# Kernel tuning notes

Hardware: AMD Instinct MI355X
Metric: run time of the kernel (lower is better)

The kernel has to match this reference:

```python
import jax, jax.numpy as jnp
import numpy as np

B, T, D, H = 2, 2048, 1024, 16
HD = D // H  # head dim = 64; rope half-dim = 32


def setup_inputs() -> dict:
    key = jax.random.key(0)
    ks = jax.random.split(key, 8)
    x = jax.random.normal(ks[0], (B, T, D), dtype=jnp.float32)
    # additive causal mask (upper triangle = -inf-like), as typically passed in
    mask = jnp.triu(jnp.full((T, T), -1e9, dtype=jnp.float32), k=1)
    # standard RoPE angles: theta = pos / 10000^(2i/hd)
    inv_freq = 1.0 / (10000.0 ** (np.arange(0, HD, 2, dtype=np.float32) / HD))
    ang = np.arange(T, dtype=np.float32)[:, None] * inv_freq[None, :]  # [T, HD//2]
    cos = jnp.asarray(np.cos(ang), dtype=jnp.float32)
    sin = jnp.asarray(np.sin(ang), dtype=jnp.float32)
    s = 1.0 / np.sqrt(D)
    Wq = jax.random.normal(ks[1], (D, D), dtype=jnp.float32) * s
    bq = jnp.zeros((D,), dtype=jnp.float32)
    Wk = jax.random.normal(ks[2], (D, D), dtype=jnp.float32) * s
    Wv = jax.random.normal(ks[3], (D, D), dtype=jnp.float32) * s
    bv = jnp.zeros((D,), dtype=jnp.float32)
    Wo = jax.random.normal(ks[4], (D, D), dtype=jnp.float32) * s
    bo = jnp.zeros((D,), dtype=jnp.float32)
    return {"x": x, "mask": mask, "cos": cos, "sin": sin, "Wq": Wq, "bq": bq,
            "Wk": Wk, "Wv": Wv, "bv": bv, "Wo": Wo, "bo": bo}


def _apply_rope(t, cos, sin):
    # t: [B, T, H, HD]; cos/sin: [T, HD//2]; complex multiply on (even, odd) pairs
    t = t.reshape(B, T, H, HD // 2, 2)
    t0, t1 = t[..., 0], t[..., 1]
    c = cos[None, :, None, :]
    s = sin[None, :, None, :]
    out = jnp.stack([t0 * c - t1 * s, t0 * s + t1 * c], axis=-1)
    return out.reshape(B, T, H, HD)


def reference(x, mask, cos, sin, Wq, bq, Wk, Wv, bv, Wo, bo):
    scale = float(HD) ** (-0.25)
    q = (x @ Wq.T + bq).reshape(B, T, H, HD)
    k = (x @ Wk.T).reshape(B, T, H, HD)  # key proj has no bias
    v = (x @ Wv.T + bv).reshape(B, T, H, HD)
    q = _apply_rope(q, cos, sin)
    k = _apply_rope(k, cos, sin)
    q = q.transpose(0, 2, 1, 3) * scale  # [B,H,T,HD]
    k = k.transpose(0, 2, 1, 3) * scale
    v = v.transpose(0, 2, 1, 3)
    qk = jnp.einsum("bhtd,bhsd->bhts", q, k) + mask  # [B,H,T,T]
    qk = qk.astype(jnp.float32)
    w = jax.nn.softmax(qk, axis=-1).astype(q.dtype)
    wv = jnp.einsum("bhts,bhsd->bhtd", w, v)
    wv = wv.transpose(0, 2, 1, 3).reshape(B, T, D)
    out = wv @ Wo.T + bo
    return out, qk
```

## Files before the change

### kernel.cpp

```cpp
#include <hip/hip_runtime.h>
#include <math.h>

#define Tc 2048
#define Dc 1024
#define Hc 16
#define HDc 64
#define BT 4096
#define SCALE 0.35355339059327379f

typedef _Float16 f16;
typedef __attribute__((ext_vector_type(4))) _Float16 f16x4;
typedef __attribute__((ext_vector_type(8))) _Float16 f16x8;
typedef __attribute__((ext_vector_type(4))) float f32x4;

__device__ __forceinline__ void gload16(const f16* g, f16* l)
{
    __builtin_amdgcn_global_load_lds(
        (const __attribute__((address_space(1))) void*)g,
        (__attribute__((address_space(3))) void*)l, 16, 0, 0);
}

template <int C>
__device__ __forceinline__ float fdpp(float x)
{
    return __int_as_float(__builtin_amdgcn_update_dpp(
        0, __float_as_int(x), C, 0xF, 0xF, true));
}
__device__ __forceinline__ float rmax16(float v)
{
    v = fmaxf(v, fdpp<0xB1>(v));
    v = fmaxf(v, fdpp<0x4E>(v));
    v = fmaxf(v, fdpp<0x124>(v));
    v = fmaxf(v, fdpp<0x128>(v));
    return v;
}
__device__ __forceinline__ float rsum16(float v)
{
    v += fdpp<0xB1>(v);
    v += fdpp<0x4E>(v);
    v += fdpp<0x124>(v);
    v += fdpp<0x128>(v);
    return v;
}

__global__ __launch_bounds__(256)
void cast_kernel(const float* __restrict__ x,
                 const float* __restrict__ Wq, const float* __restrict__ Wk,
                 const float* __restrict__ Wv, const float* __restrict__ Wo,
                 f16* __restrict__ xh,
                 f16* __restrict__ Wqh, f16* __restrict__ Wkh,
                 f16* __restrict__ Wvh, f16* __restrict__ Woh)
{
    const int u = blockIdx.y;
    const float* s; f16* d;
    if (u < 4) { s = x + (size_t)u * (1u << 20); d = xh + (size_t)u * (1u << 20); }
    else switch (u) {
        case 4:  s = Wq; d = Wqh; break;
        case 5:  s = Wk; d = Wkh; break;
        case 6:  s = Wv; d = Wvh; break;
        default: s = Wo; d = Woh; break;
    }
    int i = blockIdx.x * 256 + threadIdx.x;
    float4 v = ((const float4*)s)[i];
    f16x4 o = {(f16)v.x, (f16)v.y, (f16)v.z, (f16)v.w};
    ((f16x4*)d)[i] = o;
}

#define GEMM_BODY(Aptr, Bptr)                                                        \
    __shared__ f16 As[2][128 * 64];                                                  \
    __shared__ f16 Bs[2][64 * 64];                                                   \
    const int tid = threadIdx.x;                                                     \
    const int w = tid >> 6, l = tid & 63;                                            \
    const int lr = l & 15, lq = l >> 4;                                              \
    const int m0 = blockIdx.y * 128, n0 = blockIdx.x * 64;                           \
    const int srow8 = l >> 3, sslot = l & 7;                                         \
    f32x4 acc[2][4] = {};                                                            \
    auto STAGE = [&](int b, int k0) {                                                \
        _Pragma("unroll")                                                            \
        for (int c = 0; c < 6; c++) {                                                \
            int chunk = w * 6 + c;                                                   \
            if (chunk < 16) {                                                        \
                int row = chunk * 8 + srow8;                                         \
                int col = (sslot ^ (row & 7)) * 8;                                   \
                gload16(&Aptr[(size_t)(m0 + row) * Dc + k0 + col],                   \
                        &As[b][chunk * 512]);                                        \
            } else {                                                                 \
                int row = (chunk - 16) * 8 + srow8;                                  \
                int col = (sslot ^ (row & 7)) * 8;                                   \
                gload16(&Bptr[(size_t)(n0 + row) * Dc + k0 + col],                   \
                        &Bs[b][(chunk - 16) * 512]);                                 \
            }                                                                        \
        }                                                                            \
    };                                                                               \
    STAGE(0, 0);                                                                     \
    __syncthreads();                                                                 \
    int cur = 0;                                                                     \
    for (int k0 = 0; k0 < Dc; k0 += 64) {                                            \
        if (k0 + 64 < Dc) STAGE(cur ^ 1, k0 + 64);                                   \
        _Pragma("unroll")                                                            \
        for (int kk = 0; kk < 2; kk++) {                                             \
            f16x8 af[2], bf[4];                                                      \
            _Pragma("unroll")                                                        \
            for (int mi = 0; mi < 2; mi++) {                                         \
                int row = 32 * w + 16 * mi + lr;                                     \
                int bo = (lq * 16 + kk * 64) ^ ((row & 7) << 4);                     \
                af[mi] = *(const f16x8*)((const char*)&As[cur][0] + row * 128 + bo); \
            }                                                                        \
            _Pragma("unroll")                                                        \
            for (int ni = 0; ni < 4; ni++) {                                         \
                int row = 16 * ni + lr;                                              \
                int bo = (lq * 16 + kk * 64) ^ ((row & 7) << 4);                     \
                bf[ni] = *(const f16x8*)((const char*)&Bs[cur][0] + row * 128 + bo); \
            }                                                                        \
            _Pragma("unroll")                                                        \
            for (int mi = 0; mi < 2; mi++)                                           \
                _Pragma("unroll")                                                    \
                for (int ni = 0; ni < 4; ni++)                                       \
                    acc[mi][ni] = __builtin_amdgcn_mfma_f32_16x16x32_f16(            \
                        af[mi], bf[ni], acc[mi][ni], 0, 0, 0);                       \
        }                                                                            \
        __syncthreads();                                                             \
        cur ^= 1;                                                                    \
    }

__global__ __launch_bounds__(256, 3)
void qkv_proj_kernel(const f16* __restrict__ xh,
                     const f16* __restrict__ Wqh, const f16* __restrict__ Wkh,
                     const f16* __restrict__ Wvh,
                     const float* __restrict__ bq, const float* __restrict__ bv,
                     f16* __restrict__ qh, f16* __restrict__ kh, f16* __restrict__ vh,
                     const float* __restrict__ cosp, const float* __restrict__ sinp)
{
    const int mode = blockIdx.z;
    const f16* W = (mode == 0) ? Wqh : (mode == 1 ? Wkh : Wvh);
    const float* bias = (mode == 0) ? bq : (mode == 2 ? bv : nullptr);
    f16* dst = (mode == 0) ? qh : (mode == 1 ? kh : vh);

    GEMM_BODY(xh, W)

    #pragma unroll
    for (int mi = 0; mi < 2; mi++) {
        #pragma unroll
        for (int ni = 0; ni < 4; ni++) {
            #pragma unroll
            for (int i = 0; i < 4; i++) {
                int gm = m0 + 32 * w + 16 * mi + lq * 4 + i;
                int gn = n0 + 16 * ni + lr;
                float v = acc[mi][ni][i];
                if (bias) v += bias[gn];
                int b = gm >> 11, t = gm & 2047;
                int h = gn >> 6, d = gn & 63;
                if (mode != 2) {
                    float pv = __shfl_xor(v, 1, 64);
                    int p = d >> 1;
                    float c = cosp[t * 32 + p], s = sinp[t * 32 + p];
                    v = (d & 1) ? (pv * s + v * c) : (v * c - pv * s);
                    v *= SCALE;
                }
                dst[((size_t)(b * Hc + h) * Tc + t) * HDc + d] = (f16)v;
            }
        }
    }
}

__global__ __launch_bounds__(256, 3)
void out_proj_kernel(const f16* __restrict__ A, const f16* __restrict__ W,
                     const float* __restrict__ bias, float* __restrict__ out)
{
    GEMM_BODY(A, W)

    #pragma unroll
    for (int mi = 0; mi < 2; mi++)
        #pragma unroll
        for (int ni = 0; ni < 4; ni++)
            #pragma unroll
            for (int i = 0; i < 4; i++) {
                int gm = m0 + 32 * w + 16 * mi + lq * 4 + i;
                int gn = n0 + 16 * ni + lr;
                out[(size_t)gm * Dc + gn] = acc[mi][ni][i] + bias[gn];
            }
}

__global__ __launch_bounds__(256, 6)
void flash_kernel(const f16* __restrict__ qh, const f16* __restrict__ kh,
                  const f16* __restrict__ vh, f16* __restrict__ wvh,
                  float* __restrict__ qk)
{
    const int z = blockIdx.y;
    const int t0 = (gridDim.x - 1 - blockIdx.x) * 64;
    const int tid = threadIdx.x;
    const int w = tid >> 6, l = tid & 63;
    const int lr = l & 15, lq = l >> 4;

    __shared__ f16 Ks[64][64];
    __shared__ f16 VsT[64][68];
    __shared__ f16 Ps[64][68];

    const f16* Qg = qh + (size_t)z * Tc * HDc;
    const f16* Kg = kh + (size_t)z * Tc * HDc;
    const f16* Vg = vh + (size_t)z * Tc * HDc;
    float* C = qk + (size_t)z * Tc * Tc;

    f16x8 aq[2];
    #pragma unroll
    for (int ks = 0; ks < 2; ks++)
        aq[ks] = *(const f16x8*)&Qg[(size_t)(t0 + 16 * w + lr) * HDc + lq * 8 + 32 * ks];

    f32x4 O[4] = {};
    float mrow[4], lrow[4];
    #pragma unroll
    for (int i = 0; i < 4; i++) { mrow[i] = -1e30f; lrow[i] = 0.f; }

    const int srow8 = l >> 3, sslot = l & 7;

    for (int s0 = 0; s0 <= t0; s0 += 64) {
        __syncthreads();

        #pragma unroll
        for (int c = 0; c < 2; c++) {
            int chunk = w * 2 + c;
            int row = chunk * 8 + srow8;
            int col = (sslot ^ (row & 7)) * 8;
            gload16(&Kg[(size_t)(s0 + row) * HDc + col],
                    (f16*)((char*)&Ks[0][0] + chunk * 1024));
        }
        {
            const f16* vp = &Vg[(size_t)(s0 + l) * HDc + w * 16];
            f16x8 v0 = *(const f16x8*)vp;
            f16x8 v1 = *(const f16x8*)(vp + 8);
            #pragma unroll
            for (int j = 0; j < 8; j++) {
                VsT[w * 16 + j][l]     = v0[j];
                VsT[w * 16 + 8 + j][l] = v1[j];
            }
        }
        __syncthreads();

        f32x4 S[4] = {};
        __builtin_amdgcn_s_setprio(1);
        #pragma unroll
        for (int ks = 0; ks < 2; ks++) {
            #pragma unroll
            for (int ni = 0; ni < 4; ni++) {
                int krow = 16 * ni + lr;
                int bo = (lq * 16 + ks * 64) ^ ((krow & 7) << 4);
                f16x8 bk = *(const f16x8*)((const char*)&Ks[0][0] + krow * 128 + bo);
                S[ni] = __builtin_amdgcn_mfma_f32_16x16x32_f16(aq[ks], bk, S[ni], 0, 0, 0);
            }
        }
        __builtin_amdgcn_s_setprio(0);

        if (s0 == t0) {
            #pragma unroll
            for (int ni = 0; ni < 4; ni++)
                #pragma unroll
                for (int i = 0; i < 4; i++) {
                    int tg = t0 + 16 * w + lq * 4 + i;
                    int sg = s0 + 16 * ni + lr;
                    if (sg > tg) S[ni][i] = -1e9f;
                }
        }

        #pragma unroll
        for (int ni = 0; ni < 4; ni++)
            #pragma unroll
            for (int i = 0; i < 4; i++) {
                int tg = t0 + 16 * w + lq * 4 + i;
                int sg = s0 + 16 * ni + lr;
                C[(size_t)tg * Tc + sg] = S[ni][i];
            }

        #pragma unroll
        for (int i = 0; i < 4; i++) {
            float v = fmaxf(fmaxf(S[0][i], S[1][i]), fmaxf(S[2][i], S[3][i]));
            v = rmax16(v);
            float mnew = fmaxf(mrow[i], v);
            float alpha = __expf(mrow[i] - mnew);
            mrow[i] = mnew;
            float rs = 0.f;
            #pragma unroll
            for (int ni = 0; ni < 4; ni++) {
                float p = __expf(S[ni][i] - mnew);
                S[ni][i] = p;
                rs += p;
            }
            rs = rsum16(rs);
            lrow[i] = lrow[i] * alpha + rs;
            #pragma unroll
            for (int ni = 0; ni < 4; ni++) O[ni][i] *= alpha;
        }

        #pragma unroll
        for (int ni = 0; ni < 4; ni++)
            #pragma unroll
            for (int i = 0; i < 4; i++)
                Ps[16 * w + lq * 4 + i][16 * ni + lr] = (f16)S[ni][i];

        __builtin_amdgcn_s_setprio(1);
        #pragma unroll
        for (int ks = 0; ks < 2; ks++) {
            f16x8 ap = *(const f16x8*)&Ps[16 * w + lr][lq * 8 + 32 * ks];
            #pragma unroll
            for (int ni = 0; ni < 4; ni++) {
                f16x8 bv = *(const f16x8*)&VsT[16 * ni + lr][lq * 8 + 32 * ks];
                O[ni] = __builtin_amdgcn_mfma_f32_16x16x32_f16(ap, bv, O[ni], 0, 0, 0);
            }
        }
        __builtin_amdgcn_s_setprio(0);
    }

    const int b = z >> 4, h = z & 15;
    #pragma unroll
    for (int ni = 0; ni < 4; ni++)
        #pragma unroll
        for (int i = 0; i < 4; i++) {
            int tg = t0 + 16 * w + lq * 4 + i;
            int d = 16 * ni + lr;
            float o = O[ni][i] / lrow[i];
            wvh[((size_t)(b * Tc + tg)) * Dc + h * HDc + d] = (f16)o;
        }

    {
        int r = t0 + (tid >> 2);
        int n4 = (Tc - t0 - 64) >> 2;
        float4 mv; mv.x = mv.y = mv.z = mv.w = -1e9f;
        float4* rowp = (float4*)(C + (size_t)r * Tc + t0 + 64);
        for (int c = (tid & 3); c < n4; c += 4) rowp[c] = mv;
    }
}

extern "C" void kernel_launch(void* const* d_in, const int* in_sizes, int n_in,
                              void* d_out, int out_size, void* d_ws, size_t ws_size,
                              hipStream_t stream)
{
    const float* x    = (const float*)d_in[0];
    const float* cosp = (const float*)d_in[2];
    const float* sinp = (const float*)d_in[3];
    const float* Wq   = (const float*)d_in[4];
    const float* bq   = (const float*)d_in[5];
    const float* Wk   = (const float*)d_in[6];
    const float* Wv   = (const float*)d_in[7];
    const float* bv   = (const float*)d_in[8];
    const float* Wo   = (const float*)d_in[9];
    const float* bo   = (const float*)d_in[10];

    float* out = (float*)d_out;
    float* qk  = out + (size_t)BT * Dc;

    f16* ws  = (f16*)d_ws;
    f16* xh  = ws;
    f16* Wqh = xh  + (size_t)BT * Dc;
    f16* Wkh = Wqh + (size_t)Dc * Dc;
    f16* Wvh = Wkh + (size_t)Dc * Dc;
    f16* Woh = Wvh + (size_t)Dc * Dc;
    f16* qh  = Woh + (size_t)Dc * Dc;
    f16* kh  = qh  + (size_t)BT * Dc;
    f16* vh  = kh  + (size_t)BT * Dc;
    f16* wvh = vh  + (size_t)BT * Dc;

    dim3 blk(256);

    cast_kernel<<<dim3(1024, 8), blk, 0, stream>>>(
        x, Wq, Wk, Wv, Wo, xh, Wqh, Wkh, Wvh, Woh);

    qkv_proj_kernel<<<dim3(Dc / 64, BT / 128, 3), blk, 0, stream>>>(
        xh, Wqh, Wkh, Wvh, bq, bv, qh, kh, vh, cosp, sinp);

    flash_kernel<<<dim3(Tc / 64, 32), blk, 0, stream>>>(qh, kh, vh, wvh, qk);

    out_proj_kernel<<<dim3(Dc / 64, BT / 128), blk, 0, stream>>>(wvh, Woh, bo, out);
}
```

Before: 726.7 us.

## Split qk score output into a separate coalesced score kernel

Removes the strided scalar writes of the full qk score matrix and the masked-region fill from the flash kernel. A new score kernel recomputes Q·K^T in 128x128 tiles and stores it with vectorized f32x4 writes laid out along the key dimension. Tiles above the diagonal only write the mask constant. This recomputes the QK matmul, roughly doubling that compute, in exchange for a lighter flash loop and better-coalesced stores of the 512MB score tensor.

```diff
diff --git a/kernel.cpp b/kernel.cpp
--- a/kernel.cpp
+++ b/kernel.cpp
@@ -181,10 +181,90 @@
             }
 }
 
+__global__ __launch_bounds__(256, 4)
+void score_kernel(const f16* __restrict__ qh, const f16* __restrict__ kh,
+                  float* __restrict__ qk)
+{
+    const int z = blockIdx.z;
+    const int s0 = blockIdx.x * 128;
+    const int t0 = blockIdx.y * 128;
+    const int tid = threadIdx.x;
+    float* C = qk + (size_t)z * Tc * Tc;
+
+    if (s0 > t0) {
+        int r = t0 + (tid >> 1);
+        float* rowp = C + (size_t)r * Tc + s0 + (tid & 1) * 64;
+        f32x4 mv = {-1e9f, -1e9f, -1e9f, -1e9f};
+        #pragma unroll
+        for (int j = 0; j < 16; j++)
+            ((f32x4*)rowp)[j] = mv;
+        return;
+    }
+
+    __shared__ f16 KT[128 * 64];
+    __shared__ f16 QT[128 * 64];
+
+    const int w = tid >> 6, l = tid & 63;
+    const int lr = l & 15, lq = l >> 4;
+    const int srow8 = l >> 3, sslot = l & 7;
+
+    const f16* Qg = qh + (size_t)z * Tc * HDc;
+    const f16* Kg = kh + (size_t)z * Tc * HDc;
+
+    #pragma unroll
+    for (int c = 0; c < 8; c++) {
+        int chunk = w * 8 + c;
+        int row = (chunk & 15) * 8 + srow8;
+        int col = (sslot ^ (row & 7)) * 8;
+        if (chunk < 16)
+            gload16(&Kg[(size_t)(s0 + row) * HDc + col], &KT[chunk * 512]);
+        else
+            gload16(&Qg[(size_t)(t0 + row) * HDc + col], &QT[(chunk - 16) * 512]);
+    }
+    __syncthreads();
+
+    f32x4 acc[2][8] = {};
+    #pragma unroll
+    for (int kk = 0; kk < 2; kk++) {
+        f16x8 af[2], bf[8];
+        #pragma unroll
+        for (int mi = 0; mi < 2; mi++) {
+            int row = 32 * w + 16 * mi + lr;
+            int bo = (lq * 16 + kk * 64) ^ ((row & 7) << 4);
+            af[mi] = *(const f16x8*)((const char*)&KT[0] + row * 128 + bo);
+        }
+        #pragma unroll
+        for (int ni = 0; ni < 8; ni++) {
+            int row = 16 * ni + lr;
+            int bo = (lq * 16 + kk * 64) ^ ((row & 7) << 4);
+            bf[ni] = *(const f16x8*)((const char*)&QT[0] + row * 128 + bo);
+        }
+        #pragma unroll
+        for (int mi = 0; mi < 2; mi++)
+            #pragma unroll
+            for (int ni = 0; ni < 8; ni++)
+                acc[mi][ni] = __builtin_amdgcn_mfma_f32_16x16x32_f16(
+                    af[mi], bf[ni], acc[mi][ni], 0, 0, 0);
+    }
+
+    #pragma unroll
+    for (int mi = 0; mi < 2; mi++) {
+        int sbase = s0 + 32 * w + 16 * mi + lq * 4;
+        #pragma unroll
+        for (int ni = 0; ni < 8; ni++) {
+            int tg = t0 + 16 * ni + lr;
+            f32x4 ov = acc[mi][ni];
+            #pragma unroll
+            for (int i = 0; i < 4; i++)
+                if (sbase + i > tg) ov[i] = -1e9f;
+            *(f32x4*)(C + (size_t)tg * Tc + sbase) = ov;
+        }
+    }
+}
+
 __global__ __launch_bounds__(256, 6)
 void flash_kernel(const f16* __restrict__ qh, const f16* __restrict__ kh,
-                  const f16* __restrict__ vh, f16* __restrict__ wvh,
-                  float* __restrict__ qk)
+                  const f16* __restrict__ vh, f16* __restrict__ wvh)
 {
     const int z = blockIdx.y;
     const int t0 = (gridDim.x - 1 - blockIdx.x) * 64;
@@ -199,7 +279,6 @@
     const f16* Qg = qh + (size_t)z * Tc * HDc;
     const f16* Kg = kh + (size_t)z * Tc * HDc;
     const f16* Vg = vh + (size_t)z * Tc * HDc;
-    float* C = qk + (size_t)z * Tc * Tc;
 
     f16x8 aq[2];
     #pragma unroll
@@ -262,15 +341,6 @@
         }
 
         #pragma unroll
-        for (int ni = 0; ni < 4; ni++)
-            #pragma unroll
-            for (int i = 0; i < 4; i++) {
-                int tg = t0 + 16 * w + lq * 4 + i;
-                int sg = s0 + 16 * ni + lr;
-                C[(size_t)tg * Tc + sg] = S[ni][i];
-            }
-
-        #pragma unroll
         for (int i = 0; i < 4; i++) {
             float v = fmaxf(fmaxf(S[0][i], S[1][i]), fmaxf(S[2][i], S[3][i]));
             v = rmax16(v);
@@ -319,14 +389,6 @@
             float o = O[ni][i] / lrow[i];
             wvh[((size_t)(b * Tc + tg)) * Dc + h * HDc + d] = (f16)o;
         }
-
-    {
-        int r = t0 + (tid >> 2);
-        int n4 = (Tc - t0 - 64) >> 2;
-        float4 mv; mv.x = mv.y = mv.z = mv.w = -1e9f;
-        float4* rowp = (float4*)(C + (size_t)r * Tc + t0 + 64);
-        for (int c = (tid & 3); c < n4; c += 4) rowp[c] = mv;
-    }
 }
 
 extern "C" void kernel_launch(void* const* d_in, const int* in_sizes, int n_in,
@@ -366,7 +428,9 @@
     qkv_proj_kernel<<<dim3(Dc / 64, BT / 128, 3), blk, 0, stream>>>(
         xh, Wqh, Wkh, Wvh, bq, bv, qh, kh, vh, cosp, sinp);
 
-    flash_kernel<<<dim3(Tc / 64, 32), blk, 0, stream>>>(qh, kh, vh, wvh, qk);
+    flash_kernel<<<dim3(Tc / 64, 32), blk, 0, stream>>>(qh, kh, vh, wvh);
 
     out_proj_kernel<<<dim3(Dc / 64, BT / 128), blk, 0, stream>>>(wvh, Woh, bo, out);
-}
+
+    score_kernel<<<dim3(Tc / 128, Tc / 128, 32), blk, 0, stream>>>(qh, kh, qk);
+}
```

Result: slower. 790.8 us (+8.8%).
